# Kernel tuning notes

Hardware: AMD Instinct MI355X
Metric: run time of the kernel (lower is better)

The kernel has to match this reference:

```python
import jax, jax.numpy as jnp
import numpy as np

B, T = 16, 1024
ACTION_DIM, HIDDEN = 2048, 256
ADJ_STRENGTH = 0.1
SMOOTH = 0.9
CRIT_W = jnp.array([0.25, 0.75], dtype=jnp.float32)
NONCRIT_W = jnp.array([0.75, 0.25], dtype=jnp.float32)
LN_EPS = 1e-5


def _xavier_uniform(key, fan_in, fan_out, gain=0.1):
    limit = gain * np.sqrt(6.0 / (fan_in + fan_out))
    return jax.random.uniform(key, (fan_in, fan_out), minval=-limit, maxval=limit, dtype=jnp.float32)


def setup_inputs() -> dict:
    key = jax.random.key(0)
    ks = jax.random.split(key, 6)
    critical_labels = jax.random.randint(ks[0], (B, T), 0, 2)
    action_tokens = jax.random.normal(ks[1], (B, T, ACTION_DIM), dtype=jnp.float32)
    H2 = HIDDEN // 2
    return {
        'critical_labels': critical_labels,
        'action_tokens': action_tokens,
        'W1': _xavier_uniform(ks[2], ACTION_DIM, HIDDEN),
        'b1': jnp.zeros((HIDDEN,), jnp.float32),
        'g1': jnp.ones((HIDDEN,), jnp.float32),
        'be1': jnp.zeros((HIDDEN,), jnp.float32),
        'W2': _xavier_uniform(ks[3], HIDDEN, H2),
        'b2': jnp.zeros((H2,), jnp.float32),
        'g2': jnp.ones((H2,), jnp.float32),
        'be2': jnp.zeros((H2,), jnp.float32),
        'W3': _xavier_uniform(ks[4], H2, 2),
        'b3': jnp.zeros((2,), jnp.float32),
        'temperature': jnp.asarray(1.0, jnp.float32),
    }


def _layernorm(x, g, b):
    mu = jnp.mean(x, axis=-1, keepdims=True)
    var = jnp.var(x, axis=-1, keepdims=True)
    return (x - mu) * jax.lax.rsqrt(var + LN_EPS) * g + b


def reference(critical_labels, action_tokens, W1, b1, g1, be1, W2, b2, g2, be2, W3, b3, temperature):
    # base weights from binary labels: (B,T,2)
    crit = (critical_labels > 0)[..., None]
    base = jnp.where(crit, CRIT_W, NONCRIT_W)
    # MLP gate (dropout inactive in eval): Linear-LN-GELU x2, Linear, Tanh
    h = jax.nn.gelu(_layernorm(action_tokens @ W1 + b1, g1, be1), approximate=False)
    h = jax.nn.gelu(_layernorm(h @ W2 + b2, g2, be2), approximate=False)
    adjustments = jnp.tanh(h @ W3 + b3) * ADJ_STRENGTH
    temp = jnp.clip(temperature, 0.1, None)
    adjusted = jax.nn.softmax((base + adjustments) / temp, axis=-1)
    # temporal EMA smoothing: default state has prev_weights batch=1 != B, so t=0 passes through
    def step(s, c):
        s = SMOOTH * s + (1.0 - SMOOTH) * c
        return s, s
    init = adjusted[:, 0]                              # (B,2)
    _, rest = jax.lax.scan(step, init, jnp.swapaxes(adjusted[:, 1:], 0, 1))
    smoothed = jnp.concatenate([adjusted[:, :1], jnp.swapaxes(rest, 0, 1)], axis=1)
    return smoothed
```

## Files before the change

kernel.cpp:

```cpp
#include <hip/hip_runtime.h>
#include <hip/hip_bf16.h>
#include <math.h>

typedef __bf16 bf16x8 __attribute__((ext_vector_type(8)));
typedef float  f32x4  __attribute__((ext_vector_type(4)));

#define MFMA16(a,b,c) __builtin_amdgcn_mfma_f32_16x16x32_bf16(a,b,c,0,0,0)

__device__ __forceinline__ float gelu_exact(float x){
    return 0.5f * x * (1.0f + erff(x * 0.7071067811865476f));
}

__device__ __forceinline__ void gld_lds16(const void* g, void* l){
    __builtin_amdgcn_global_load_lds(
        (const __attribute__((address_space(1))) unsigned int*)g,
        (__attribute__((address_space(3))) unsigned int*)l, 16, 0, 0);
}

__global__ void transp_bf16(const float* __restrict__ src, __bf16* __restrict__ dst,
                            int K, int N){
    int k0 = blockIdx.x * 8;
    int n  = threadIdx.x;
    if (n >= N) return;
    bf16x8 v;
#pragma unroll
    for (int r = 0; r < 8; ++r)
        v[r] = (__bf16)src[(size_t)(k0 + r) * N + n];
    *(bf16x8*)&dst[(size_t)n * K + k0] = v;
}

__global__ __launch_bounds__(512, 1) void gemm1_ln_gelu(
    const float* __restrict__ X, const __bf16* __restrict__ W1T,
    const float* __restrict__ b1, const float* __restrict__ g1,
    const float* __restrict__ be1, __bf16* __restrict__ H1)
{
    __shared__ __bf16 lA[3][64*64];
    __shared__ __bf16 lB[3][256*64];
    __shared__ float  redS[64][4];
    __shared__ float  redQ[64][4];

    const int tid  = threadIdx.x;
    const int wid  = tid >> 6;
    const int lane = tid & 63;
    const int l15  = lane & 15;
    const int lg   = lane >> 4;
    const int wm   = wid >> 2;
    const int wn   = wid & 3;
    const int mBase = blockIdx.x * 64;

    const int sRow = tid >> 3;
    const int sC8  = (tid & 7) * 8;
    const int sDst = sRow * 64 + (sC8 ^ ((sRow & 7) << 3));
    const float* aSrc = X + (size_t)(mBase + sRow) * 2048 + sC8;

    const __bf16* bSrc[4];
    int ldsOff[4];
#pragma unroll
    for (int r = 0; r < 4; ++r){
        int j   = wid*256 + r*64 + lane;
        int row = j >> 3;
        int c   = (j & 7) ^ (row & 7);
        bSrc[r] = W1T + (size_t)row * 2048 + c*8;
        ldsOff[r] = __builtin_amdgcn_readfirstlane(wid*4096 + r*1024);
    }

    f32x4 acc[2][4] = {};
    float4 pA0, pA1, nA0, nA1;

#define WRITEA(BUF, A0_, A1_) {                                              \
        bf16x8 v;                                                            \
        v[0]=(__bf16)A0_.x; v[1]=(__bf16)A0_.y; v[2]=(__bf16)A0_.z;          \
        v[3]=(__bf16)A0_.w; v[4]=(__bf16)A1_.x; v[5]=(__bf16)A1_.y;          \
        v[6]=(__bf16)A1_.z; v[7]=(__bf16)A1_.w;                              \
        *(bf16x8*)&lA[BUF][sDst] = v; }

#define STAGEB(BUF, KT) {                                                    \
        char* _lb = (char*)&lB[BUF][0];                                      \
        _Pragma("unroll")                                                    \
        for (int r = 0; r < 4; ++r)                                          \
            gld_lds16(bSrc[r] + (KT)*64, _lb + ldsOff[r]); }

#define COMPUTE(BUF) {                                                       \
        const __bf16* pa = &lA[BUF][0];                                      \
        const __bf16* pb = &lB[BUF][0];                                      \
        _Pragma("unroll")                                                    \
        for (int kk = 0; kk < 2; ++kk){                                      \
            const int kx = (kk*32 + lg*8) ^ ((l15 & 7) << 3);                \
            bf16x8 av0 = *(const bf16x8*)&pa[(wm*32      + l15)*64 + kx];    \
            bf16x8 av1 = *(const bf16x8*)&pa[(wm*32 + 16 + l15)*64 + kx];    \
            bf16x8 bv0 = *(const bf16x8*)&pb[(wn*64      + l15)*64 + kx];    \
            bf16x8 bv1 = *(const bf16x8*)&pb[(wn*64 + 16 + l15)*64 + kx];    \
            bf16x8 bv2 = *(const bf16x8*)&pb[(wn*64 + 32 + l15)*64 + kx];    \
            bf16x8 bv3 = *(const bf16x8*)&pb[(wn*64 + 48 + l15)*64 + kx];    \
            acc[0][0] = MFMA16(av0, bv0, acc[0][0]);                         \
            acc[0][1] = MFMA16(av0, bv1, acc[0][1]);                         \
            acc[0][2] = MFMA16(av0, bv2, acc[0][2]);                         \
            acc[0][3] = MFMA16(av0, bv3, acc[0][3]);                         \
            acc[1][0] = MFMA16(av1, bv0, acc[1][0]);                         \
            acc[1][1] = MFMA16(av1, bv1, acc[1][1]);                         \
            acc[1][2] = MFMA16(av1, bv2, acc[1][2]);                         \
            acc[1][3] = MFMA16(av1, bv3, acc[1][3]);                         \
        } }

#define STEP(P0, P1, N0, N1)                                                 \
    {                                                                        \
        int bw = bc + 1; if (bw >= 3) bw -= 3;                               \
        int bn = bc + 2; if (bn >= 3) bn -= 3;                               \
        N0 = *(const float4*)(aSrc + (size_t)(t+2)*64);                      \
        N1 = *(const float4*)(aSrc + (size_t)(t+2)*64 + 4);                  \
        __builtin_amdgcn_sched_barrier(0);                                   \
        STAGEB(bn, t+2);                                                     \
        __builtin_amdgcn_sched_barrier(0);                                   \
        COMPUTE(bc);                                                         \
        __builtin_amdgcn_sched_barrier(0);                                   \
        WRITEA(bw, P0, P1);                                                  \
        asm volatile("s_waitcnt vmcnt(6) lgkmcnt(0)" ::: "memory");          \
        __builtin_amdgcn_s_barrier();                                        \
        __builtin_amdgcn_sched_barrier(0);                                   \
        bc = bw; ++t;                                                        \
    }

    pA0 = *(const float4*)(aSrc);
    pA1 = *(const float4*)(aSrc + 4);
    __builtin_amdgcn_sched_barrier(0);
    STAGEB(0, 0);
    __builtin_amdgcn_sched_barrier(0);
    WRITEA(0, pA0, pA1);
    pA0 = *(const float4*)(aSrc + 64);
    pA1 = *(const float4*)(aSrc + 64 + 4);
    __builtin_amdgcn_sched_barrier(0);
    STAGEB(1, 1);
    __builtin_amdgcn_sched_barrier(0);
    asm volatile("s_waitcnt vmcnt(6) lgkmcnt(0)" ::: "memory");
    __builtin_amdgcn_s_barrier();
    __builtin_amdgcn_sched_barrier(0);

    int t = 0, bc = 0;
    for (int it = 0; it < 15; ++it){
        STEP(pA0, pA1, nA0, nA1);
        STEP(nA0, nA1, pA0, pA1);
    }
    COMPUTE(0);
    __builtin_amdgcn_sched_barrier(0);
    WRITEA(1, pA0, pA1);
    asm volatile("s_waitcnt vmcnt(0) lgkmcnt(0)" ::: "memory");
    __builtin_amdgcn_s_barrier();
    __builtin_amdgcn_sched_barrier(0);
    COMPUTE(1);

    float bias_[4], g1_[4], be_[4];
#pragma unroll
    for (int n = 0; n < 4; ++n){
        int col = wn*64 + n*16 + l15;
        bias_[n] = b1[col]; g1_[n] = g1[col]; be_[n] = be1[col];
    }
#pragma unroll
    for (int m = 0; m < 2; ++m)
#pragma unroll
        for (int n = 0; n < 4; ++n)
#pragma unroll
            for (int r = 0; r < 4; ++r)
                acc[m][n][r] += bias_[n];

#pragma unroll
    for (int m = 0; m < 2; ++m)
#pragma unroll
        for (int r = 0; r < 4; ++r){
            float s = 0.f, q = 0.f;
#pragma unroll
            for (int n = 0; n < 4; ++n){ float v = acc[m][n][r]; s += v; q += v*v; }
#pragma unroll
            for (int off = 1; off <= 8; off <<= 1){
                s += __shfl_xor(s, off, 64);
                q += __shfl_xor(q, off, 64);
            }
            int row = wm*32 + m*16 + lg*4 + r;
            if (l15 == 0){ redS[row][wn] = s; redQ[row][wn] = q; }
        }
    __syncthreads();

#pragma unroll
    for (int m = 0; m < 2; ++m)
#pragma unroll
        for (int r = 0; r < 4; ++r){
            int row = wm*32 + m*16 + lg*4 + r;
            float su = redS[row][0]+redS[row][1]+redS[row][2]+redS[row][3];
            float qu = redQ[row][0]+redQ[row][1]+redQ[row][2]+redQ[row][3];
            float mu  = su * (1.f/256.f);
            float var = qu * (1.f/256.f) - mu*mu;
            float rs  = rsqrtf(var + 1e-5f);
            size_t base = (size_t)(mBase + row) * 256;
#pragma unroll
            for (int n = 0; n < 4; ++n){
                float x  = acc[m][n][r];
                float xn = (x - mu) * rs * g1_[n] + be_[n];
                H1[base + wn*64 + n*16 + l15] = (__bf16)gelu_exact(xn);
            }
        }
#undef WRITEA
#undef STAGEB
#undef COMPUTE
#undef STEP
}

__global__ __launch_bounds__(512) void tail_fused(
    const __bf16* __restrict__ H1, const __bf16* __restrict__ W2T,
    const float* __restrict__ b2, const float* __restrict__ g2,
    const float* __restrict__ be2, const float* __restrict__ W3,
    const float* __restrict__ b3, const int* __restrict__ labels,
    const float* __restrict__ temperature, float* __restrict__ ADJ)
{
    __shared__ union { __bf16 lH[64*256]; float h2[64*128]; } u;
    __shared__ __bf16 lW[128*256];
    __shared__ float  redS[64][4];
    __shared__ float  redQ[64][4];
    __shared__ float  lw3[256];

    const int tid  = threadIdx.x;
    const int wid  = tid >> 6;
    const int lane = tid & 63;
    const int l15  = lane & 15;
    const int lg   = lane >> 4;
    const int wm   = wid >> 2, wn = wid & 3;
    const int mBase = blockIdx.x * 64;

    {
        int r0 = tid >> 5;
        int c8 = (tid & 31) * 8;
        int swz = c8 ^ ((r0 & 7) << 3);
#pragma unroll
        for (int i = 0; i < 4; ++i){
            int row = r0 + i*16;
            bf16x8 v = *(const bf16x8*)&H1[(size_t)(mBase+row)*256 + c8];
            *(bf16x8*)&u.lH[row*256 + swz] = v;
        }
#pragma unroll
        for (int i = 0; i < 8; ++i){
            int row = r0 + i*16;
            bf16x8 v = *(const bf16x8*)&W2T[(size_t)row*256 + c8];
            *(bf16x8*)&lW[row*256 + swz] = v;
        }
        if (tid < 256) lw3[tid] = W3[tid];
    }
    __syncthreads();

    f32x4 acc[2][2] = {};
#pragma unroll
    for (int kk = 0; kk < 8; ++kk){
        const int kcol = kk*32 + lg*8;
        bf16x8 av[2], bv[2];
#pragma unroll
        for (int m = 0; m < 2; ++m){
            int row = wm*32 + m*16 + l15;
            av[m] = *(const bf16x8*)&u.lH[row*256 + (kcol ^ ((row&7)<<3))];
        }
#pragma unroll
        for (int n = 0; n < 2; ++n){
            int row = wn*32 + n*16 + l15;
            bv[n] = *(const bf16x8*)&lW[row*256 + (kcol ^ ((row&7)<<3))];
        }
#pragma unroll
        for (int m = 0; m < 2; ++m)
#pragma unroll
            for (int n = 0; n < 2; ++n)
                acc[m][n] = MFMA16(av[m], bv[n], acc[m][n]);
    }

    float b2_[2], g2_[2], be_[2];
#pragma unroll
    for (int n = 0; n < 2; ++n){
        int col = wn*32 + n*16 + l15;
        b2_[n] = b2[col]; g2_[n] = g2[col]; be_[n] = be2[col];
    }
#pragma unroll
    for (int m = 0; m < 2; ++m)
#pragma unroll
        for (int n = 0; n < 2; ++n)
#pragma unroll
            for (int r = 0; r < 4; ++r)
                acc[m][n][r] += b2_[n];

#pragma unroll
    for (int m = 0; m < 2; ++m)
#pragma unroll
        for (int r = 0; r < 4; ++r){
            float s = 0.f, q = 0.f;
#pragma unroll
            for (int n = 0; n < 2; ++n){ float v = acc[m][n][r]; s += v; q += v*v; }
#pragma unroll
            for (int off = 1; off <= 8; off <<= 1){
                s += __shfl_xor(s, off, 64);
                q += __shfl_xor(q, off, 64);
            }
            int row = wm*32 + m*16 + lg*4 + r;
            if (l15 == 0){ redS[row][wn] = s; redQ[row][wn] = q; }
        }
    __syncthreads();

#pragma unroll
    for (int m = 0; m < 2; ++m)
#pragma unroll
        for (int r = 0; r < 4; ++r){
            int row = wm*32 + m*16 + lg*4 + r;
            float su = redS[row][0]+redS[row][1]+redS[row][2]+redS[row][3];
            float qu = redQ[row][0]+redQ[row][1]+redQ[row][2]+redQ[row][3];
            float mu  = su * (1.f/128.f);
            float var = qu * (1.f/128.f) - mu*mu;
            float rs  = rsqrtf(var + 1e-5f);
#pragma unroll
            for (int n = 0; n < 2; ++n){
                int col = wn*32 + n*16 + l15;
                float x = acc[m][n][r];
                float h = gelu_exact((x - mu)*rs*g2_[n] + be_[n]);
                u.h2[row*128 + (col ^ (row & 31))] = h;
            }
        }
    __syncthreads();

    if (tid < 64){
        const int row = tid;
        const int g = mBase + row;
        float a0 = b3[0], a1 = b3[1];
        for (int k = 0; k < 128; ++k){
            float v = u.h2[row*128 + (k ^ (row & 31))];
            a0 += v * lw3[2*k];
            a1 += v * lw3[2*k+1];
        }
        float t = fmaxf(temperature[0], 0.1f);
        float adj0 = tanhf(a0) * 0.1f;
        float adj1 = tanhf(a1) * 0.1f;
        bool crit = labels[g] > 0;
        float base0 = crit ? 0.25f : 0.75f;
        float base1 = crit ? 0.75f : 0.25f;
        float L0 = (base0 + adj0) / t, L1 = (base1 + adj1) / t;
        float mm = fmaxf(L0, L1);
        float e0 = expf(L0 - mm), e1 = expf(L1 - mm);
        float inv = 1.f / (e0 + e1);
        ADJ[(size_t)g*2    ] = e0 * inv;
        ADJ[(size_t)g*2 + 1] = e1 * inv;
    }
}

__global__ void ema_kernel(const float* __restrict__ ADJ, float* __restrict__ out)
{
    __shared__ float wtab[128];
    __shared__ float abuf[384*2];
    const int b     = blockIdx.x >> 2;
    const int chunk = blockIdx.x & 3;
    const int c0    = chunk * 256;
    const int tid   = threadIdx.x;
    if (tid < 128) wtab[tid] = powf(0.9f, (float)tid);
    for (int idx = tid; idx < 768; idx += 256){
        int tt = c0 - 128 + (idx >> 1);
        int cc = idx & 1;
        abuf[idx] = (tt >= 0) ? ADJ[((size_t)b*1024 + tt)*2 + cc] : 0.f;
    }
    __syncthreads();
#pragma unroll
    for (int i = 0; i < 2; ++i){
        int item = tid + i*256;
        int tl = item >> 1, cc = item & 1;
        int t = c0 + tl;
        int kmax = min(t, 127);
        float sum = 0.f;
        for (int k = 0; k <= kmax; ++k){
            float coef = (t - k == 0) ? wtab[k] : 0.1f * wtab[k];
            sum += coef * abuf[(tl - k + 128)*2 + cc];
        }
        out[((size_t)b*1024 + t)*2 + cc] = sum;
    }
}

extern "C" void kernel_launch(void* const* d_in, const int* in_sizes, int n_in,
                              void* d_out, int out_size, void* d_ws, size_t ws_size,
                              hipStream_t stream)
{
    const int*   labels = (const int*)  d_in[0];
    const float* X      = (const float*)d_in[1];
    const float* W1     = (const float*)d_in[2];
    const float* b1     = (const float*)d_in[3];
    const float* g1     = (const float*)d_in[4];
    const float* be1    = (const float*)d_in[5];
    const float* W2     = (const float*)d_in[6];
    const float* b2     = (const float*)d_in[7];
    const float* g2     = (const float*)d_in[8];
    const float* be2    = (const float*)d_in[9];
    const float* W3     = (const float*)d_in[10];
    const float* b3     = (const float*)d_in[11];
    const float* temp   = (const float*)d_in[12];
    float* out = (float*)d_out;

    char* ws = (char*)d_ws;
    __bf16* W1T = (__bf16*)(ws);
    __bf16* W2T = (__bf16*)(ws + 1048576);
    __bf16* H1  = (__bf16*)(ws + 1114112);
    float*  ADJ = (float*)(ws + 9502720);

    transp_bf16<<<256, 256, 0, stream>>>(W1, W1T, 2048, 256);
    transp_bf16<<<32,  256, 0, stream>>>(W2, W2T, 256, 128);
    gemm1_ln_gelu<<<256, 512, 0, stream>>>(X, W1T, b1, g1, be1, H1);
    tail_fused<<<256, 512, 0, stream>>>(H1, W2T, b2, g2, be2, W3, b3, labels, temp, ADJ);
    ema_kernel<<<64, 256, 0, stream>>>(ADJ, out);
}
```

Baseline: 86.84 us.

## Shrink GEMM1 tile to 32 rows by 32 K and launch 512 blocks

The first GEMM+LayerNorm+GELU kernel now works on 32-row M tiles with a K step of 32 instead of 64x64, which doubles the grid to 512 blocks so all CUs get work. Launch bounds now allow several blocks per CU. The LDS swizzle is rewritten for the narrower rows, and the pipeline's wait counts and loop count are updated to match. The cost is that every block reloads the full W1 slice for half as many rows, and each MFMA step does less work per barrier, so there are more synchronisation points.

```diff
diff --git a/kernel.cpp b/kernel.cpp
--- a/kernel.cpp
+++ b/kernel.cpp
@@ -3,9 +3,11 @@
 #include <math.h>
 
 typedef __bf16 bf16x8 __attribute__((ext_vector_type(8)));
+typedef __bf16 bf16x2 __attribute__((ext_vector_type(2)));
 typedef float  f32x4  __attribute__((ext_vector_type(4)));
 
 #define MFMA16(a,b,c) __builtin_amdgcn_mfma_f32_16x16x32_bf16(a,b,c,0,0,0)
+#define PHI(r) ((((r) + ((r) >> 2))) & 3)
 
 __device__ __forceinline__ float gelu_exact(float x){
     return 0.5f * x * (1.0f + erff(x * 0.7071067811865476f));
@@ -29,15 +31,15 @@
     *(bf16x8*)&dst[(size_t)n * K + k0] = v;
 }
 
-__global__ __launch_bounds__(512, 1) void gemm1_ln_gelu(
+__global__ __launch_bounds__(512, 4) void gemm1_ln_gelu(
     const float* __restrict__ X, const __bf16* __restrict__ W1T,
     const float* __restrict__ b1, const float* __restrict__ g1,
     const float* __restrict__ be1, __bf16* __restrict__ H1)
 {
-    __shared__ __bf16 lA[3][64*64];
-    __shared__ __bf16 lB[3][256*64];
-    __shared__ float  redS[64][4];
-    __shared__ float  redQ[64][4];
+    __shared__ __bf16 lA[3][32*32];
+    __shared__ __bf16 lB[3][256*32];
+    __shared__ float  redS[32][4];
+    __shared__ float  redQ[32][4];
 
     const int tid  = threadIdx.x;
     const int wid  = tid >> 6;
@@ -46,107 +48,99 @@
     const int lg   = lane >> 4;
     const int wm   = wid >> 2;
     const int wn   = wid & 3;
-    const int mBase = blockIdx.x * 64;
-
-    const int sRow = tid >> 3;
-    const int sC8  = (tid & 7) * 8;
-    const int sDst = sRow * 64 + (sC8 ^ ((sRow & 7) << 3));
-    const float* aSrc = X + (size_t)(mBase + sRow) * 2048 + sC8;
-
-    const __bf16* bSrc[4];
-    int ldsOff[4];
-#pragma unroll
-    for (int r = 0; r < 4; ++r){
-        int j   = wid*256 + r*64 + lane;
-        int row = j >> 3;
-        int c   = (j & 7) ^ (row & 7);
-        bSrc[r] = W1T + (size_t)row * 2048 + c*8;
-        ldsOff[r] = __builtin_amdgcn_readfirstlane(wid*4096 + r*1024);
-    }
-
-    f32x4 acc[2][4] = {};
-    float4 pA0, pA1, nA0, nA1;
-
-#define WRITEA(BUF, A0_, A1_) {                                              \
-        bf16x8 v;                                                            \
-        v[0]=(__bf16)A0_.x; v[1]=(__bf16)A0_.y; v[2]=(__bf16)A0_.z;          \
-        v[3]=(__bf16)A0_.w; v[4]=(__bf16)A1_.x; v[5]=(__bf16)A1_.y;          \
-        v[6]=(__bf16)A1_.z; v[7]=(__bf16)A1_.w;                              \
-        *(bf16x8*)&lA[BUF][sDst] = v; }
+    const int mBase = blockIdx.x * 32;
+
+    const int sRow = tid >> 4;
+    const int sC2  = (tid & 15) * 2;
+    const int sDst = sRow * 32 + (sC2 ^ (PHI(sRow) << 3));
+    const float* aSrc = X + (size_t)(mBase + sRow) * 2048 + sC2;
+
+    const __bf16* bSrc[2];
+    int ldsOff[2];
+#pragma unroll
+    for (int r = 0; r < 2; ++r){
+        int j    = wid*128 + r*64 + lane;
+        int row  = j >> 2;
+        int slot = j & 3;
+        int c    = slot ^ PHI(row);
+        bSrc[r]  = W1T + (size_t)row * 2048 + c*8;
+        ldsOff[r] = __builtin_amdgcn_readfirstlane(wid*2048 + r*1024);
+    }
+
+    f32x4 acc[4] = {};
+    float2 pA, nA;
+
+#define WRITEA(BUF, P_) {                                                    \
+        bf16x2 v; v[0] = (__bf16)P_.x; v[1] = (__bf16)P_.y;                  \
+        *(bf16x2*)&lA[BUF][sDst] = v; }
 
 #define STAGEB(BUF, KT) {                                                    \
         char* _lb = (char*)&lB[BUF][0];                                      \
         _Pragma("unroll")                                                    \
-        for (int r = 0; r < 4; ++r)                                          \
-            gld_lds16(bSrc[r] + (KT)*64, _lb + ldsOff[r]); }
+        for (int r = 0; r < 2; ++r)                                          \
+            gld_lds16(bSrc[r] + (size_t)(KT)*32, _lb + ldsOff[r]); }
 
 #define COMPUTE(BUF) {                                                       \
         const __bf16* pa = &lA[BUF][0];                                      \
         const __bf16* pb = &lB[BUF][0];                                      \
-        _Pragma("unroll")                                                    \
-        for (int kk = 0; kk < 2; ++kk){                                      \
-            const int kx = (kk*32 + lg*8) ^ ((l15 & 7) << 3);                \
-            bf16x8 av0 = *(const bf16x8*)&pa[(wm*32      + l15)*64 + kx];    \
-            bf16x8 av1 = *(const bf16x8*)&pa[(wm*32 + 16 + l15)*64 + kx];    \
-            bf16x8 bv0 = *(const bf16x8*)&pb[(wn*64      + l15)*64 + kx];    \
-            bf16x8 bv1 = *(const bf16x8*)&pb[(wn*64 + 16 + l15)*64 + kx];    \
-            bf16x8 bv2 = *(const bf16x8*)&pb[(wn*64 + 32 + l15)*64 + kx];    \
-            bf16x8 bv3 = *(const bf16x8*)&pb[(wn*64 + 48 + l15)*64 + kx];    \
-            acc[0][0] = MFMA16(av0, bv0, acc[0][0]);                         \
-            acc[0][1] = MFMA16(av0, bv1, acc[0][1]);                         \
-            acc[0][2] = MFMA16(av0, bv2, acc[0][2]);                         \
-            acc[0][3] = MFMA16(av0, bv3, acc[0][3]);                         \
-            acc[1][0] = MFMA16(av1, bv0, acc[1][0]);                         \
-            acc[1][1] = MFMA16(av1, bv1, acc[1][1]);                         \
-            acc[1][2] = MFMA16(av1, bv2, acc[1][2]);                         \
-            acc[1][3] = MFMA16(av1, bv3, acc[1][3]);                         \
-        } }
-
-#define STEP(P0, P1, N0, N1)                                                 \
+        const int ar = wm*16 + l15;                                          \
+        bf16x8 av = *(const bf16x8*)&pa[ar*32 + ((lg*8) ^ (PHI(ar)<<3))];    \
+        const int br0 = wn*64      + l15;                                    \
+        const int br1 = wn*64 + 16 + l15;                                    \
+        const int br2 = wn*64 + 32 + l15;                                    \
+        const int br3 = wn*64 + 48 + l15;                                    \
+        bf16x8 bv0 = *(const bf16x8*)&pb[br0*32 + ((lg*8) ^ (PHI(br0)<<3))]; \
+        bf16x8 bv1 = *(const bf16x8*)&pb[br1*32 + ((lg*8) ^ (PHI(br1)<<3))]; \
+        bf16x8 bv2 = *(const bf16x8*)&pb[br2*32 + ((lg*8) ^ (PHI(br2)<<3))]; \
+        bf16x8 bv3 = *(const bf16x8*)&pb[br3*32 + ((lg*8) ^ (PHI(br3)<<3))]; \
+        acc[0] = MFMA16(av, bv0, acc[0]);                                    \
+        acc[1] = MFMA16(av, bv1, acc[1]);                                    \
+        acc[2] = MFMA16(av, bv2, acc[2]);                                    \
+        acc[3] = MFMA16(av, bv3, acc[3]);                                    \
+    }
+
+#define STEP(P_, N_)                                                         \
     {                                                                        \
         int bw = bc + 1; if (bw >= 3) bw -= 3;                               \
         int bn = bc + 2; if (bn >= 3) bn -= 3;                               \
-        N0 = *(const float4*)(aSrc + (size_t)(t+2)*64);                      \
-        N1 = *(const float4*)(aSrc + (size_t)(t+2)*64 + 4);                  \
+        N_ = *(const float2*)(aSrc + (size_t)(t+2)*32);                      \
         __builtin_amdgcn_sched_barrier(0);                                   \
         STAGEB(bn, t+2);                                                     \
         __builtin_amdgcn_sched_barrier(0);                                   \
         COMPUTE(bc);                                                         \
         __builtin_amdgcn_sched_barrier(0);                                   \
-        WRITEA(bw, P0, P1);                                                  \
-        asm volatile("s_waitcnt vmcnt(6) lgkmcnt(0)" ::: "memory");          \
+        WRITEA(bw, P_);                                                      \
+        asm volatile("s_waitcnt vmcnt(3) lgkmcnt(0)" ::: "memory");          \
         __builtin_amdgcn_s_barrier();                                        \
         __builtin_amdgcn_sched_barrier(0);                                   \
         bc = bw; ++t;                                                        \
     }
 
-    pA0 = *(const float4*)(aSrc);
-    pA1 = *(const float4*)(aSrc + 4);
+    pA = *(const float2*)(aSrc);
     __builtin_amdgcn_sched_barrier(0);
     STAGEB(0, 0);
     __builtin_amdgcn_sched_barrier(0);
-    WRITEA(0, pA0, pA1);
-    pA0 = *(const float4*)(aSrc + 64);
-    pA1 = *(const float4*)(aSrc + 64 + 4);
+    WRITEA(0, pA);
+    pA = *(const float2*)(aSrc + 32);
     __builtin_amdgcn_sched_barrier(0);
     STAGEB(1, 1);
     __builtin_amdgcn_sched_barrier(0);
-    asm volatile("s_waitcnt vmcnt(6) lgkmcnt(0)" ::: "memory");
+    asm volatile("s_waitcnt vmcnt(3) lgkmcnt(0)" ::: "memory");
     __builtin_amdgcn_s_barrier();
     __builtin_amdgcn_sched_barrier(0);
 
     int t = 0, bc = 0;
-    for (int it = 0; it < 15; ++it){
-        STEP(pA0, pA1, nA0, nA1);
-        STEP(nA0, nA1, pA0, pA1);
-    }
-    COMPUTE(0);
-    __builtin_amdgcn_sched_barrier(0);
-    WRITEA(1, pA0, pA1);
+    for (int it = 0; it < 31; ++it){
+        STEP(pA, nA);
+        STEP(nA, pA);
+    }
+    COMPUTE(2);
+    __builtin_amdgcn_sched_barrier(0);
+    WRITEA(0, pA);
     asm volatile("s_waitcnt vmcnt(0) lgkmcnt(0)" ::: "memory");
     __builtin_amdgcn_s_barrier();
     __builtin_amdgcn_sched_barrier(0);
-    COMPUTE(1);
+    COMPUTE(0);
 
     float bias_[4], g1_[4], be_[4];
 #pragma unroll
@@ -155,48 +149,42 @@
         bias_[n] = b1[col]; g1_[n] = g1[col]; be_[n] = be1[col];
     }
 #pragma unroll
-    for (int m = 0; m < 2; ++m)
-#pragma unroll
-        for (int n = 0; n < 4; ++n)
-#pragma unroll
-            for (int r = 0; r < 4; ++r)
-                acc[m][n][r] += bias_[n];
-
-#pragma unroll
-    for (int m = 0; m < 2; ++m)
-#pragma unroll
-        for (int r = 0; r < 4; ++r){
-            float s = 0.f, q = 0.f;
-#pragma unroll
-            for (int n = 0; n < 4; ++n){ float v = acc[m][n][r]; s += v; q += v*v; }
-#pragma unroll
-            for (int off = 1; off <= 8; off <<= 1){
-                s += __shfl_xor(s, off, 64);
-                q += __shfl_xor(q, off, 64);
-            }
-            int row = wm*32 + m*16 + lg*4 + r;
-            if (l15 == 0){ redS[row][wn] = s; redQ[row][wn] = q; }
-        }
-    __syncthreads();
-
-#pragma unroll
-    for (int m = 0; m < 2; ++m)
-#pragma unroll
-        for (int r = 0; r < 4; ++r){
-            int row = wm*32 + m*16 + lg*4 + r;
-            float su = redS[row][0]+redS[row][1]+redS[row][2]+redS[row][3];
-            float qu = redQ[row][0]+redQ[row][1]+redQ[row][2]+redQ[row][3];
-            float mu  = su * (1.f/256.f);
-            float var = qu * (1.f/256.f) - mu*mu;
-            float rs  = rsqrtf(var + 1e-5f);
-            size_t base = (size_t)(mBase + row) * 256;
-#pragma unroll
-            for (int n = 0; n < 4; ++n){
-                float x  = acc[m][n][r];
-                float xn = (x - mu) * rs * g1_[n] + be_[n];
-                H1[base + wn*64 + n*16 + l15] = (__bf16)gelu_exact(xn);
-            }
-        }
+    for (int n = 0; n < 4; ++n)
+#pragma unroll
+        for (int r = 0; r < 4; ++r)
+            acc[n][r] += bias_[n];
+
+#pragma unroll
+    for (int r = 0; r < 4; ++r){
+        float s = 0.f, q = 0.f;
+#pragma unroll
+        for (int n = 0; n < 4; ++n){ float v = acc[n][r]; s += v; q += v*v; }
+#pragma unroll
+        for (int off = 1; off <= 8; off <<= 1){
+            s += __shfl_xor(s, off, 64);
+            q += __shfl_xor(q, off, 64);
+        }
+        int row = wm*16 + lg*4 + r;
+        if (l15 == 0){ redS[row][wn] = s; redQ[row][wn] = q; }
+    }
+    __syncthreads();
+
+#pragma unroll
+    for (int r = 0; r < 4; ++r){
+        int row = wm*16 + lg*4 + r;
+        float su = redS[row][0]+redS[row][1]+redS[row][2]+redS[row][3];
+        float qu = redQ[row][0]+redQ[row][1]+redQ[row][2]+redQ[row][3];
+        float mu  = su * (1.f/256.f);
+        float var = qu * (1.f/256.f) - mu*mu;
+        float rs  = rsqrtf(var + 1e-5f);
+        size_t base = (size_t)(mBase + row) * 256;
+#pragma unroll
+        for (int n = 0; n < 4; ++n){
+            float x  = acc[n][r];
+            float xn = (x - mu) * rs * g1_[n] + be_[n];
+            H1[base + wn*64 + n*16 + l15] = (__bf16)gelu_exact(xn);
+        }
+    }
 #undef WRITEA
 #undef STAGEB
 #undef COMPUTE
@@ -398,7 +386,7 @@
 
     transp_bf16<<<256, 256, 0, stream>>>(W1, W1T, 2048, 256);
     transp_bf16<<<32,  256, 0, stream>>>(W2, W2T, 256, 128);
-    gemm1_ln_gelu<<<256, 512, 0, stream>>>(X, W1T, b1, g1, be1, H1);
+    gemm1_ln_gelu<<<512, 512, 0, stream>>>(X, W1T, b1, g1, be1, H1);
     tail_fused<<<256, 512, 0, stream>>>(H1, W2T, b2, g2, be2, W3, b3, labels, temp, ADJ);
     ema_kernel<<<64, 256, 0, stream>>>(ADJ, out);
 }
```

New measurement: 88.86 us. 1.02x slower.

## Split GEMM1 along K into two partials with 128-row tiles, add LN/GELU kernel

Applied to the files above, without the earlier changes.

GEMM1 now uses 128x256 output tiles, so each W1 tile loaded into LDS is reused across twice as many rows, and the K dimension is split in half across paired blocks to keep 256 blocks. Each half writes a bf16 partial sum to separate buffers. A new kernel adds the two partials plus bias, then applies LayerNorm and exact GELU. This cuts redundant W1 traffic per row, at the cost of an extra launch, extra global round-trips of partials, and rounding partial sums to bf16 before they are added.

```diff
diff --git a/kernel.cpp b/kernel.cpp
--- a/kernel.cpp
+++ b/kernel.cpp
@@ -3,6 +3,7 @@
 #include <math.h>
 
 typedef __bf16 bf16x8 __attribute__((ext_vector_type(8)));
+typedef __bf16 bf16x4 __attribute__((ext_vector_type(4)));
 typedef float  f32x4  __attribute__((ext_vector_type(4)));
 
 #define MFMA16(a,b,c) __builtin_amdgcn_mfma_f32_16x16x32_bf16(a,b,c,0,0,0)
@@ -29,15 +30,12 @@
     *(bf16x8*)&dst[(size_t)n * K + k0] = v;
 }
 
-__global__ __launch_bounds__(512, 1) void gemm1_ln_gelu(
+__global__ __launch_bounds__(512, 1) void gemm1_pre(
     const float* __restrict__ X, const __bf16* __restrict__ W1T,
-    const float* __restrict__ b1, const float* __restrict__ g1,
-    const float* __restrict__ be1, __bf16* __restrict__ H1)
+    __bf16* __restrict__ H1p)
 {
-    __shared__ __bf16 lA[3][64*64];
+    __shared__ __bf16 lA[2][128*64];
     __shared__ __bf16 lB[3][256*64];
-    __shared__ float  redS[64][4];
-    __shared__ float  redQ[64][4];
 
     const int tid  = threadIdx.x;
     const int wid  = tid >> 6;
@@ -46,161 +44,164 @@
     const int lg   = lane >> 4;
     const int wm   = wid >> 2;
     const int wn   = wid & 3;
-    const int mBase = blockIdx.x * 64;
-
-    const int sRow = tid >> 3;
-    const int sC8  = (tid & 7) * 8;
-    const int sDst = sRow * 64 + (sC8 ^ ((sRow & 7) << 3));
-    const float* aSrc = X + (size_t)(mBase + sRow) * 2048 + sC8;
+    const int mBase = (blockIdx.x >> 1) * 128;
+    const int kBlk  = blockIdx.x & 1;
+    const int kBase = kBlk << 10;
+
+    const int sRow = tid >> 2;
+    const int sQ   = (tid & 3) * 16;
+    const int swzA = (sRow & 7) << 3;
+    const float* aSrc = X + (size_t)(mBase + sRow) * 2048 + kBase + sQ;
 
     const __bf16* bSrc[4];
     int ldsOff[4];
 #pragma unroll
     for (int r = 0; r < 4; ++r){
-        int j   = wid*256 + r*64 + lane;
+        int j   = tid + r*512;
         int row = j >> 3;
         int c   = (j & 7) ^ (row & 7);
-        bSrc[r] = W1T + (size_t)row * 2048 + c*8;
-        ldsOff[r] = __builtin_amdgcn_readfirstlane(wid*4096 + r*1024);
-    }
-
-    f32x4 acc[2][4] = {};
-    float4 pA0, pA1, nA0, nA1;
-
-#define WRITEA(BUF, A0_, A1_) {                                              \
-        bf16x8 v;                                                            \
-        v[0]=(__bf16)A0_.x; v[1]=(__bf16)A0_.y; v[2]=(__bf16)A0_.z;          \
-        v[3]=(__bf16)A0_.w; v[4]=(__bf16)A1_.x; v[5]=(__bf16)A1_.y;          \
-        v[6]=(__bf16)A1_.z; v[7]=(__bf16)A1_.w;                              \
-        *(bf16x8*)&lA[BUF][sDst] = v; }
+        bSrc[r] = W1T + (size_t)row * 2048 + kBase + c*8;
+        ldsOff[r] = __builtin_amdgcn_readfirstlane(wid*1024 + r*8192);
+    }
+
+    f32x4 acc[4][4] = {};
+    float4 pA[4], nA[4];
+
+#define ISSUEA(BANK, T) {                                                    \
+        _Pragma("unroll")                                                    \
+        for (int i = 0; i < 4; ++i)                                          \
+            BANK[i] = *(const float4*)(aSrc + (size_t)(T)*64 + i*4); }
 
 #define STAGEB(BUF, KT) {                                                    \
         char* _lb = (char*)&lB[BUF][0];                                      \
         _Pragma("unroll")                                                    \
         for (int r = 0; r < 4; ++r)                                          \
-            gld_lds16(bSrc[r] + (KT)*64, _lb + ldsOff[r]); }
-
-#define COMPUTE(BUF) {                                                       \
-        const __bf16* pa = &lA[BUF][0];                                      \
-        const __bf16* pb = &lB[BUF][0];                                      \
+            gld_lds16(bSrc[r] + (size_t)(KT)*64, _lb + ldsOff[r]); }
+
+#define WRITEA(BUF, BANK) {                                                  \
+        bf16x8 v0, v1;                                                       \
+        v0[0]=(__bf16)BANK[0].x; v0[1]=(__bf16)BANK[0].y;                    \
+        v0[2]=(__bf16)BANK[0].z; v0[3]=(__bf16)BANK[0].w;                    \
+        v0[4]=(__bf16)BANK[1].x; v0[5]=(__bf16)BANK[1].y;                    \
+        v0[6]=(__bf16)BANK[1].z; v0[7]=(__bf16)BANK[1].w;                    \
+        v1[0]=(__bf16)BANK[2].x; v1[1]=(__bf16)BANK[2].y;                    \
+        v1[2]=(__bf16)BANK[2].z; v1[3]=(__bf16)BANK[2].w;                    \
+        v1[4]=(__bf16)BANK[3].x; v1[5]=(__bf16)BANK[3].y;                    \
+        v1[6]=(__bf16)BANK[3].z; v1[7]=(__bf16)BANK[3].w;                    \
+        *(bf16x8*)&lA[BUF][sRow*64 + ( sQ      ^ swzA)] = v0;                \
+        *(bf16x8*)&lA[BUF][sRow*64 + ((sQ + 8) ^ swzA)] = v1; }
+
+#define COMPUTE(CA, CB) {                                                    \
         _Pragma("unroll")                                                    \
         for (int kk = 0; kk < 2; ++kk){                                      \
             const int kx = (kk*32 + lg*8) ^ ((l15 & 7) << 3);                \
-            bf16x8 av0 = *(const bf16x8*)&pa[(wm*32      + l15)*64 + kx];    \
-            bf16x8 av1 = *(const bf16x8*)&pa[(wm*32 + 16 + l15)*64 + kx];    \
-            bf16x8 bv0 = *(const bf16x8*)&pb[(wn*64      + l15)*64 + kx];    \
-            bf16x8 bv1 = *(const bf16x8*)&pb[(wn*64 + 16 + l15)*64 + kx];    \
-            bf16x8 bv2 = *(const bf16x8*)&pb[(wn*64 + 32 + l15)*64 + kx];    \
-            bf16x8 bv3 = *(const bf16x8*)&pb[(wn*64 + 48 + l15)*64 + kx];    \
-            acc[0][0] = MFMA16(av0, bv0, acc[0][0]);                         \
-            acc[0][1] = MFMA16(av0, bv1, acc[0][1]);                         \
-            acc[0][2] = MFMA16(av0, bv2, acc[0][2]);                         \
-            acc[0][3] = MFMA16(av0, bv3, acc[0][3]);                         \
-            acc[1][0] = MFMA16(av1, bv0, acc[1][0]);                         \
-            acc[1][1] = MFMA16(av1, bv1, acc[1][1]);                         \
-            acc[1][2] = MFMA16(av1, bv2, acc[1][2]);                         \
-            acc[1][3] = MFMA16(av1, bv3, acc[1][3]);                         \
+            bf16x8 av[4], bv[4];                                             \
+            _Pragma("unroll")                                                \
+            for (int m = 0; m < 4; ++m)                                      \
+                av[m] = *(const bf16x8*)&lA[CA][(wm*64 + m*16 + l15)*64 + kx]; \
+            _Pragma("unroll")                                                \
+            for (int n = 0; n < 4; ++n)                                      \
+                bv[n] = *(const bf16x8*)&lB[CB][(wn*64 + n*16 + l15)*64 + kx]; \
+            _Pragma("unroll")                                                \
+            for (int m = 0; m < 4; ++m)                                      \
+                _Pragma("unroll")                                            \
+                for (int n = 0; n < 4; ++n)                                  \
+                    acc[m][n] = MFMA16(av[m], bv[n], acc[m][n]);             \
         } }
 
-#define STEP(P0, P1, N0, N1)                                                 \
+#define STEP(PB, NB)                                                         \
     {                                                                        \
-        int bw = bc + 1; if (bw >= 3) bw -= 3;                               \
         int bn = bc + 2; if (bn >= 3) bn -= 3;                               \
-        N0 = *(const float4*)(aSrc + (size_t)(t+2)*64);                      \
-        N1 = *(const float4*)(aSrc + (size_t)(t+2)*64 + 4);                  \
+        ISSUEA(NB, t+2);                                                     \
         __builtin_amdgcn_sched_barrier(0);                                   \
         STAGEB(bn, t+2);                                                     \
         __builtin_amdgcn_sched_barrier(0);                                   \
-        COMPUTE(bc);                                                         \
+        COMPUTE(t & 1, bc);                                                  \
         __builtin_amdgcn_sched_barrier(0);                                   \
-        WRITEA(bw, P0, P1);                                                  \
-        asm volatile("s_waitcnt vmcnt(6) lgkmcnt(0)" ::: "memory");          \
+        WRITEA((t+1) & 1, PB);                                               \
+        asm volatile("s_waitcnt vmcnt(8) lgkmcnt(0)" ::: "memory");          \
         __builtin_amdgcn_s_barrier();                                        \
         __builtin_amdgcn_sched_barrier(0);                                   \
-        bc = bw; ++t;                                                        \
-    }
-
-    pA0 = *(const float4*)(aSrc);
-    pA1 = *(const float4*)(aSrc + 4);
+        bc = bc + 1; if (bc >= 3) bc -= 3;                                   \
+        ++t;                                                                 \
+    }
+
+    ISSUEA(pA, 0);
     __builtin_amdgcn_sched_barrier(0);
     STAGEB(0, 0);
     __builtin_amdgcn_sched_barrier(0);
-    WRITEA(0, pA0, pA1);
-    pA0 = *(const float4*)(aSrc + 64);
-    pA1 = *(const float4*)(aSrc + 64 + 4);
+    WRITEA(0, pA);
+    ISSUEA(pA, 1);
     __builtin_amdgcn_sched_barrier(0);
     STAGEB(1, 1);
     __builtin_amdgcn_sched_barrier(0);
-    asm volatile("s_waitcnt vmcnt(6) lgkmcnt(0)" ::: "memory");
+    asm volatile("s_waitcnt vmcnt(8) lgkmcnt(0)" ::: "memory");
     __builtin_amdgcn_s_barrier();
     __builtin_amdgcn_sched_barrier(0);
 
     int t = 0, bc = 0;
-    for (int it = 0; it < 15; ++it){
-        STEP(pA0, pA1, nA0, nA1);
-        STEP(nA0, nA1, pA0, pA1);
-    }
-    COMPUTE(0);
-    __builtin_amdgcn_sched_barrier(0);
-    WRITEA(1, pA0, pA1);
+    for (int it = 0; it < 7; ++it){
+        STEP(pA, nA);
+        STEP(nA, pA);
+    }
+    COMPUTE(0, 2);
+    __builtin_amdgcn_sched_barrier(0);
+    WRITEA(1, pA);
     asm volatile("s_waitcnt vmcnt(0) lgkmcnt(0)" ::: "memory");
     __builtin_amdgcn_s_barrier();
     __builtin_amdgcn_sched_barrier(0);
-    COMPUTE(1);
-
-    float bias_[4], g1_[4], be_[4];
-#pragma unroll
-    for (int n = 0; n < 4; ++n){
-        int col = wn*64 + n*16 + l15;
-        bias_[n] = b1[col]; g1_[n] = g1[col]; be_[n] = be1[col];
-    }
-#pragma unroll
-    for (int m = 0; m < 2; ++m)
-#pragma unroll
-        for (int n = 0; n < 4; ++n)
-#pragma unroll
-            for (int r = 0; r < 4; ++r)
-                acc[m][n][r] += bias_[n];
-
-#pragma unroll
-    for (int m = 0; m < 2; ++m)
+    COMPUTE(1, 0);
+
+    __bf16* dst = H1p + (size_t)kBlk * 16384 * 256;
+#pragma unroll
+    for (int m = 0; m < 4; ++m)
 #pragma unroll
         for (int r = 0; r < 4; ++r){
-            float s = 0.f, q = 0.f;
-#pragma unroll
-            for (int n = 0; n < 4; ++n){ float v = acc[m][n][r]; s += v; q += v*v; }
-#pragma unroll
-            for (int off = 1; off <= 8; off <<= 1){
-                s += __shfl_xor(s, off, 64);
-                q += __shfl_xor(q, off, 64);
+            size_t row = (size_t)(mBase + wm*64 + m*16 + lg*4 + r);
+#pragma unroll
+            for (int n = 0; n < 4; ++n){
+                int col = wn*64 + n*16 + l15;
+                dst[row*256 + col] = (__bf16)acc[m][n][r];
             }
-            int row = wm*32 + m*16 + lg*4 + r;
-            if (l15 == 0){ redS[row][wn] = s; redQ[row][wn] = q; }
-        }
-    __syncthreads();
-
-#pragma unroll
-    for (int m = 0; m < 2; ++m)
-#pragma unroll
-        for (int r = 0; r < 4; ++r){
-            int row = wm*32 + m*16 + lg*4 + r;
-            float su = redS[row][0]+redS[row][1]+redS[row][2]+redS[row][3];
-            float qu = redQ[row][0]+redQ[row][1]+redQ[row][2]+redQ[row][3];
-            float mu  = su * (1.f/256.f);
-            float var = qu * (1.f/256.f) - mu*mu;
-            float rs  = rsqrtf(var + 1e-5f);
-            size_t base = (size_t)(mBase + row) * 256;
-#pragma unroll
-            for (int n = 0; n < 4; ++n){
-                float x  = acc[m][n][r];
-                float xn = (x - mu) * rs * g1_[n] + be_[n];
-                H1[base + wn*64 + n*16 + l15] = (__bf16)gelu_exact(xn);
-            }
-        }
+        }
+#undef ISSUEA
+#undef STAGEB
 #undef WRITEA
-#undef STAGEB
 #undef COMPUTE
 #undef STEP
+}
+
+__global__ __launch_bounds__(512) void ln_gelu_k(
+    const __bf16* __restrict__ pA_, __bf16* __restrict__ pB_,
+    const float* __restrict__ b1, const float* __restrict__ g1,
+    const float* __restrict__ be1)
+{
+    const int row  = blockIdx.x * 8 + (threadIdx.x >> 6);
+    const int lane = threadIdx.x & 63;
+    const int c0   = lane * 4;
+
+    bf16x4 a = *(const bf16x4*)&pA_[(size_t)row*256 + c0];
+    bf16x4 b = *(const bf16x4*)&pB_[(size_t)row*256 + c0];
+    float x[4];
+    float s = 0.f, q = 0.f;
+#pragma unroll
+    for (int e = 0; e < 4; ++e){
+        x[e] = (float)a[e] + (float)b[e] + b1[c0 + e];
+        s += x[e]; q += x[e]*x[e];
+    }
+#pragma unroll
+    for (int off = 1; off <= 32; off <<= 1){
+        s += __shfl_xor(s, off, 64);
+        q += __shfl_xor(q, off, 64);
+    }
+    float mu  = s * (1.f/256.f);
+    float var = q * (1.f/256.f) - mu*mu;
+    float rs  = rsqrtf(var + 1e-5f);
+    bf16x4 o;
+#pragma unroll
+    for (int e = 0; e < 4; ++e)
+        o[e] = (__bf16)gelu_exact((x[e] - mu) * rs * g1[c0 + e] + be1[c0 + e]);
+    *(bf16x4*)&pB_[(size_t)row*256 + c0] = o;
 }
 
 __global__ __launch_bounds__(512) void tail_fused(
@@ -391,14 +392,16 @@
     float* out = (float*)d_out;
 
     char* ws = (char*)d_ws;
-    __bf16* W1T = (__bf16*)(ws);
-    __bf16* W2T = (__bf16*)(ws + 1048576);
-    __bf16* H1  = (__bf16*)(ws + 1114112);
-    float*  ADJ = (float*)(ws + 9502720);
+    __bf16* W1T  = (__bf16*)(ws);
+    __bf16* W2T  = (__bf16*)(ws + 1048576);
+    __bf16* H1pA = (__bf16*)(ws + 1114112);
+    __bf16* H1pB = (__bf16*)(ws + 9502720);
+    float*  ADJ  = (float*)(ws + 17891328);
 
     transp_bf16<<<256, 256, 0, stream>>>(W1, W1T, 2048, 256);
     transp_bf16<<<32,  256, 0, stream>>>(W2, W2T, 256, 128);
-    gemm1_ln_gelu<<<256, 512, 0, stream>>>(X, W1T, b1, g1, be1, H1);
-    tail_fused<<<256, 512, 0, stream>>>(H1, W2T, b2, g2, be2, W3, b3, labels, temp, ADJ);
+    gemm1_pre<<<256, 512, 0, stream>>>(X, W1T, H1pA);
+    ln_gelu_k<<<2048, 512, 0, stream>>>(H1pA, H1pB, b1, g1, be1);
+    tail_fused<<<256, 512, 0, stream>>>(H1pB, W2T, b2, g2, be2, W3, b3, labels, temp, ADJ);
     ema_kernel<<<64, 256, 0, stream>>>(ADJ, out);
 }
```

Result: no change. 86.83 us (-0.0%).
